# Optimization experiments

Measured on AMD Instinct MI355X. Metric: run time of the kernel, lower is better.

Reference implementation:

```python
import jax, jax.numpy as jnp
import numpy as np

S, T, I = 4096, 64, 64          # spatial cells, timesteps, input features
EH, E, H = 128, 256, 512        # embedding hidden, embedding size, LSTM hidden
LG, O, F1, F2 = 32, 128, 256, 64


def setup_inputs() -> dict:
    key = jax.random.key(0)
    ks = jax.random.split(key, 24)
    w = lambda k, shape: jax.random.normal(k, shape, jnp.float32) * 0.05
    return {
        "inputData": jax.random.normal(ks[0], (S, T, I), jnp.float32),
        "lane": jax.random.uniform(ks[1], (1, 1), jnp.float32),
        # lane gate MLP
        "Wlg1": w(ks[2], (LG, 1)),  "blg1": w(ks[3], (LG,)),
        "Wlg2": w(ks[4], (1, LG)),  "blg2": w(ks[5], (1,)),
        # embedding MLP
        "We1": w(ks[6], (EH, I)),   "be1": w(ks[7], (EH,)),
        "We2": w(ks[8], (E, EH)),   "be2": w(ks[9], (E,)),
        # LSTMCell params (torch layout: [4H, in]/[4H, H], gate order i,f,g,o)
        "Wih": w(ks[10], (4 * H, E)), "bih": w(ks[11], (4 * H,)),
        "Whh": w(ks[12], (4 * H, H)), "bhh": w(ks[13], (4 * H,)),
        # output head
        "Wout": w(ks[14], (O, H)),  "bout": w(ks[15], (O,)),
        "Wf1": w(ks[16], (F1, O)),  "bf1": w(ks[17], (F1,)),
        "Wf2": w(ks[18], (F2, F1)), "bf2": w(ks[19], (F2,)),
        "Wf3": w(ks[20], (1, F2)),  "bf3": w(ks[21], (1,)),
    }


def _spatial_maxpool(h):
    # MaxPool1d(kernel=3, stride=1, padding=1) over the spatial axis (axis 0),
    # implicit -inf padding as in torch maxpool.
    hp = jnp.pad(h, ((1, 1), (0, 0)), constant_values=-jnp.inf)
    return jnp.maximum(jnp.maximum(hp[:-2], hp[1:-1]), hp[2:])


def reference(inputData, lane, Wlg1, blg1, Wlg2, blg2, We1, be1, We2, be2,
              Wih, bih, Whh, bhh, Wout, bout, Wf1, bf1, Wf2, bf2, Wf3, bf3):
    # lane gate -> scalar in (0,1)
    lg = jax.nn.relu(lane @ Wlg1.T + blg1)
    laneC = jax.nn.sigmoid(lg @ Wlg2.T + blg2)          # [1,1]
    x = inputData * laneC.reshape(1, 1, 1)              # [S,T,I]
    # embedding MLP
    x = jax.nn.relu(x @ We1.T + be1)
    x = jax.nn.relu(x @ We2.T + be2)                    # [S,T,E]
    xt = jnp.transpose(x, (1, 0, 2))                    # [T,S,E]

    def step(carry, x_t):
        h, c = carry
        gates = x_t @ Wih.T + bih + h @ Whh.T + bhh     # [S,4H]
        i, f, g, o = jnp.split(gates, 4, axis=-1)
        c = jax.nn.sigmoid(f) * c + jax.nn.sigmoid(i) * jnp.tanh(g)
        h = jax.nn.sigmoid(o) * jnp.tanh(c)
        h = _spatial_maxpool(h)
        return (h, c), None

    h0 = jnp.zeros((inputData.shape[0], H), jnp.float32)
    c0 = jnp.zeros((inputData.shape[0], H), jnp.float32)
    (h, c), _ = jax.lax.scan(step, (h0, c0), xt)

    out = h @ Wout.T + bout
    out = jax.nn.relu(out @ Wf1.T + bf1)
    out = jax.nn.relu(out @ Wf2.T + bf2)
    out = out @ Wf3.T + bf3                             # [S,1]
    out = out / laneC.reshape(-1, 1)
    return (out, h, c)
```

## Files before the change

### kernel.cpp

```cpp
#include <hip/hip_runtime.h>
#include <hip/hip_bf16.h>
#include <cstdint>
#include <cstddef>

using bf16 = __hip_bfloat16;

typedef __attribute__((ext_vector_type(8))) short s8vec;
typedef __attribute__((ext_vector_type(4))) float f4vec;

#define SD 4096
#define TD 64
#define ID 64
#define EHD 128
#define ED 256
#define HD 512
#define GD 2048
#define OD 128
#define F1D 256
#define F2D 64

__device__ __forceinline__ float sigmf(float x) { return 1.0f / (1.0f + __expf(-x)); }
__device__ __forceinline__ float tanh_fast(float x) { return 1.0f - 2.0f / (__expf(2.0f * x) + 1.0f); }

__device__ __forceinline__ void async16(const bf16* g, void* lds) {
    __builtin_amdgcn_global_load_lds(
        (const __attribute__((address_space(1))) void*)g,
        (__attribute__((address_space(3))) void*)lds, 16, 0, 0);
}

constexpr int MODE_BF16 = 0;
constexpr int MODE_SCATTER = 2;
constexpr int MODE_LSTM = 3;

template <int MODE>
__global__ __launch_bounds__(256, 2)
void gemm_kernel(const bf16* __restrict__ A1, int lda1,
                 const bf16* __restrict__ A2, int lda2, int ksplit,
                 const bf16* __restrict__ B, int ldb,
                 const float* __restrict__ bias,
                 const float* __restrict__ scale,
                 int relu, void* __restrict__ Cp, int ldc,
                 int K, int ncols,
                 const float* __restrict__ c_in, float* __restrict__ c_out,
                 bf16* __restrict__ h_pre)
{
    __shared__ __align__(16) bf16 As[128 * 64];
    __shared__ __align__(16) bf16 Bs[128 * 64];

    const int tid = threadIdx.x;
    const int lane = tid & 63;
    const int w = tid >> 6;
    const int wm = w & 1, wn = w >> 1;
    const int m0 = blockIdx.x * 128, n0 = blockIdx.y * 128;
    const int lm = lane & 15, lq = lane >> 4;

    f4vec acc[4][4];
#pragma unroll
    for (int i = 0; i < 4; ++i)
#pragma unroll
        for (int j = 0; j < 4; ++j) acc[i][j] = (f4vec){0.f, 0.f, 0.f, 0.f};

    for (int kc = 0; kc < K; kc += 64) {
        const bf16* Ab;
        int Alda, kk;
        if (kc < ksplit) { Ab = A1; Alda = lda1; kk = kc; }
        else             { Ab = A2; Alda = lda2; kk = kc - ksplit; }

#pragma unroll
        for (int it = 0; it < 4; ++it) {
            int flat = it * 256 + tid;
            int row = flat >> 3, colu = flat & 7;
            const bf16* ga = Ab + (size_t)(m0 + row) * Alda + kk + colu * 8;
            const bf16* gb = B + (size_t)(n0 + row) * ldb + kc + colu * 8;
            uint32_t off = (uint32_t)(it * 256 + (tid & ~63)) * 16u;
            async16(ga, (char*)As + off);
            async16(gb, (char*)Bs + off);
        }
        __syncthreads();

#pragma unroll
        for (int ks = 0; ks < 64; ks += 32) {
            s8vec af[4], bfr[4];
#pragma unroll
            for (int mi = 0; mi < 4; ++mi)
                af[mi] = *(const s8vec*)(As + (wm * 64 + mi * 16 + lm) * 64 + ks + lq * 8);
#pragma unroll
            for (int ni = 0; ni < 4; ++ni)
                bfr[ni] = *(const s8vec*)(Bs + (wn * 64 + ni * 16 + lm) * 64 + ks + lq * 8);
#pragma unroll
            for (int mi = 0; mi < 4; ++mi)
#pragma unroll
                for (int ni = 0; ni < 4; ++ni)
                    acc[mi][ni] = __builtin_amdgcn_mfma_f32_16x16x32_bf16(af[mi], bfr[ni], acc[mi][ni], 0, 0, 0);
        }
        __syncthreads();
    }

    if constexpr (MODE == MODE_LSTM) {
        const int j = (n0 >> 2) + wn * 16 + lm;
        const float bi = bias[n0 + wn * 64 + lm];
        const float bff = bias[n0 + wn * 64 + 16 + lm];
        const float bg = bias[n0 + wn * 64 + 32 + lm];
        const float bo = bias[n0 + wn * 64 + 48 + lm];
#pragma unroll
        for (int mi = 0; mi < 4; ++mi) {
#pragma unroll
            for (int r = 0; r < 4; ++r) {
                const int row = m0 + wm * 64 + mi * 16 + lq * 4 + r;
                float gi = acc[mi][0][r] + bi;
                float gf = acc[mi][1][r] + bff;
                float gg = acc[mi][2][r] + bg;
                float go = acc[mi][3][r] + bo;
                float cn = sigmf(gf) * c_in[(size_t)row * HD + j] + sigmf(gi) * tanh_fast(gg);
                c_out[(size_t)row * HD + j] = cn;
                h_pre[(size_t)row * HD + j] = __float2bfloat16(sigmf(go) * tanh_fast(cn));
            }
        }
        return;
    }

    const float sc = scale ? scale[0] : 1.0f;
#pragma unroll
    for (int mi = 0; mi < 4; ++mi) {
#pragma unroll
        for (int ni = 0; ni < 4; ++ni) {
            const int gcol = n0 + wn * 64 + ni * 16 + lm;
            const float bv = bias[gcol];
#pragma unroll
            for (int r = 0; r < 4; ++r) {
                const int grow = m0 + wm * 64 + mi * 16 + lq * 4 + r;
                float v = acc[mi][ni][r] * sc + bv;
                if (relu) v = fmaxf(v, 0.f);
                if constexpr (MODE == MODE_BF16) {
                    if (gcol < ncols)
                        ((bf16*)Cp)[(size_t)grow * ldc + gcol] = __float2bfloat16(v);
                } else {
                    const int crow = (grow & 63) * SD + (grow >> 6);
                    ((bf16*)Cp)[(size_t)crow * ldc + gcol] = __float2bfloat16(v);
                }
            }
        }
    }
}

__global__ void prep_kernel(const float* __restrict__ Wih, const float* __restrict__ Whh,
                            const float* __restrict__ bih, const float* __restrict__ bhh,
                            const float* __restrict__ We1, const float* __restrict__ We2,
                            const float* __restrict__ Wout, const float* __restrict__ Wf1,
                            const float* __restrict__ Wf2, const float* __restrict__ bf2,
                            bf16* __restrict__ Wpack, float* __restrict__ biasg,
                            bf16* __restrict__ We1b, bf16* __restrict__ We2b,
                            bf16* __restrict__ Woutb, bf16* __restrict__ Wf1b,
                            bf16* __restrict__ Wf2p, float* __restrict__ bf2f)
{
    int idx = blockIdx.x * 256 + threadIdx.x;
    const int S0 = GD * (ED + HD);
    if (idx < S0) {
        int p = idx / (ED + HD), k = idx - p * (ED + HD);
        int q = p & 127;
        int j = (p >> 7) * 32 + ((q >> 6) << 4) + (q & 15);
        int gate = (q >> 4) & 3;
        int orig = gate * HD + j;
        float v = (k < ED) ? Wih[(size_t)orig * ED + k] : Whh[(size_t)orig * HD + (k - ED)];
        Wpack[idx] = __float2bfloat16(v);
        return;
    }
    idx -= S0;
    if (idx < GD) {
        int p = idx, q = p & 127;
        int j = (p >> 7) * 32 + ((q >> 6) << 4) + (q & 15);
        int gate = (q >> 4) & 3;
        int orig = gate * HD + j;
        biasg[p] = bih[orig] + bhh[orig];
        return;
    }
    idx -= GD;
    if (idx < EHD * ID) { We1b[idx] = __float2bfloat16(We1[idx]); return; }
    idx -= EHD * ID;
    if (idx < ED * EHD) { We2b[idx] = __float2bfloat16(We2[idx]); return; }
    idx -= ED * EHD;
    if (idx < OD * HD) { Woutb[idx] = __float2bfloat16(Wout[idx]); return; }
    idx -= OD * HD;
    if (idx < F1D * OD) { Wf1b[idx] = __float2bfloat16(Wf1[idx]); return; }
    idx -= F1D * OD;
    if (idx < 128 * F1D) {
        int nrow = idx >> 8;
        Wf2p[idx] = (nrow < F2D) ? __float2bfloat16(Wf2[idx]) : __float2bfloat16(0.f);
        return;
    }
    idx -= 128 * F1D;
    if (idx < 128) { bf2f[idx] = (idx < F2D) ? bf2[idx] : 0.f; return; }
}

__global__ void cvt_input_kernel(const float* __restrict__ src, bf16* __restrict__ dst)
{
    int i = (blockIdx.x * 256 + threadIdx.x) * 8;
    float4 a = *(const float4*)(src + i);
    float4 b = *(const float4*)(src + i + 4);
    bf16 o[8] = { __float2bfloat16(a.x), __float2bfloat16(a.y),
                  __float2bfloat16(a.z), __float2bfloat16(a.w),
                  __float2bfloat16(b.x), __float2bfloat16(b.y),
                  __float2bfloat16(b.z), __float2bfloat16(b.w) };
    *(uint4*)(dst + i) = *(const uint4*)o;
}

__global__ void lane_kernel(const float* __restrict__ lane, const float* __restrict__ Wlg1,
                            const float* __restrict__ blg1, const float* __restrict__ Wlg2,
                            const float* __restrict__ blg2, float* __restrict__ laneC)
{
    if (threadIdx.x != 0) return;
    const float l = lane[0];
    float acc = blg2[0];
    for (int k = 0; k < 32; ++k)
        acc += fmaxf(l * Wlg1[k] + blg1[k], 0.f) * Wlg2[k];
    float v = 1.f / (1.f + __expf(-acc));
    laneC[0] = v;
    laneC[1] = 1.f / v;
}

__global__ void zero_kernel(float* __restrict__ c0, bf16* __restrict__ h)
{
    int idx = blockIdx.x * 256 + threadIdx.x;
    if (idx < SD * HD) { c0[idx] = 0.f; h[idx] = __float2bfloat16(0.f); }
}

__global__ void maxpool_kernel(const bf16* __restrict__ hp, bf16* __restrict__ hout)
{
    int base = (blockIdx.x * 256 + threadIdx.x) * 8;
    int s = base >> 9;
    const uint4 vm = *(const uint4*)(hp + base);
    const unsigned short* m = (const unsigned short*)&vm;
    uint4 vu, vd;
    const unsigned short* u = nullptr; const unsigned short* d = nullptr;
    if (s > 0)      { vu = *(const uint4*)(hp + base - HD); u = (const unsigned short*)&vu; }
    if (s < SD - 1) { vd = *(const uint4*)(hp + base + HD); d = (const unsigned short*)&vd; }
    unsigned short o[8];
#pragma unroll
    for (int e = 0; e < 8; ++e) {
        float v = __bfloat162float(__ushort_as_bfloat16(m[e]));
        if (u) v = fmaxf(v, __bfloat162float(__ushort_as_bfloat16(u[e])));
        if (d) v = fmaxf(v, __bfloat162float(__ushort_as_bfloat16(d[e])));
        o[e] = __bfloat16_as_ushort(__float2bfloat16(v));
    }
    *(uint4*)(hout + base) = *(const uint4*)o;
}

__global__ void f3_kernel(const bf16* __restrict__ xf2, const float* __restrict__ Wf3,
                          const float* __restrict__ bf3, const float* __restrict__ laneC,
                          float* __restrict__ out)
{
    int s = blockIdx.x * 256 + threadIdx.x;
    if (s >= SD) return;
    float acc = bf3[0];
#pragma unroll
    for (int k = 0; k < F2D; ++k)
        acc += __bfloat162float(xf2[(size_t)s * F2D + k]) * Wf3[k];
    out[s] = acc * laneC[1];
}

__global__ void finalize_kernel(const bf16* __restrict__ h, const float* __restrict__ c,
                                float* __restrict__ out)
{
    int idx = blockIdx.x * 256 + threadIdx.x;
    if (idx >= SD * HD) return;
    out[SD + idx] = __bfloat162float(h[idx]);
    out[SD + SD * HD + idx] = c[idx];
}

extern "C" void kernel_launch(void* const* d_in, const int* in_sizes, int n_in,
                              void* d_out, int out_size, void* d_ws, size_t ws_size,
                              hipStream_t stream)
{
    (void)in_sizes; (void)n_in; (void)out_size;
    const float* inputDataF = (const float*)d_in[0];
    const float* lane = (const float*)d_in[1];
    const float* Wlg1 = (const float*)d_in[2];
    const float* blg1 = (const float*)d_in[3];
    const float* Wlg2 = (const float*)d_in[4];
    const float* blg2 = (const float*)d_in[5];
    const float* We1 = (const float*)d_in[6];
    const float* be1 = (const float*)d_in[7];
    const float* We2 = (const float*)d_in[8];
    const float* be2 = (const float*)d_in[9];
    const float* Wih = (const float*)d_in[10];
    const float* bih = (const float*)d_in[11];
    const float* Whh = (const float*)d_in[12];
    const float* bhh = (const float*)d_in[13];
    const float* Wout = (const float*)d_in[14];
    const float* bout = (const float*)d_in[15];
    const float* Wf1 = (const float*)d_in[16];
    const float* bf1 = (const float*)d_in[17];
    const float* Wf2 = (const float*)d_in[18];
    const float* bf2 = (const float*)d_in[19];
    const float* Wf3 = (const float*)d_in[20];
    const float* bf3 = (const float*)d_in[21];
    float* out = (float*)d_out;

    char* wp = (char*)d_ws;
    auto carve = [&](size_t bytes) { char* p = wp; wp += (bytes + 255) & ~(size_t)255; return p; };

    bf16* inb   = (bf16*)carve((size_t)SD * TD * ID * 2);
    float* laneCbuf = (float*)carve(2 * sizeof(float));
    float* cbuf0 = (float*)carve((size_t)SD * HD * 4);
    float* cbuf1 = (float*)carve((size_t)SD * HD * 4);
    bf16* hbuf  = (bf16*)carve((size_t)SD * HD * 2);
    bf16* hpre  = (bf16*)carve((size_t)SD * HD * 2);
    bf16* Wpack = (bf16*)carve((size_t)GD * (ED + HD) * 2);
    float* biasg = (float*)carve(GD * 4);
    float* bf2f = (float*)carve(128 * 4);
    bf16* We1b  = (bf16*)carve((size_t)EHD * ID * 2);
    bf16* We2b  = (bf16*)carve((size_t)ED * EHD * 2);
    bf16* Woutb = (bf16*)carve((size_t)OD * HD * 2);
    bf16* Wf1b  = (bf16*)carve((size_t)F1D * OD * 2);
    bf16* Wf2p  = (bf16*)carve((size_t)128 * F1D * 2);
    bf16* out_o = (bf16*)carve((size_t)SD * OD * 2);
    bf16* xf1   = (bf16*)carve((size_t)SD * F1D * 2);
    bf16* xf2   = (bf16*)carve((size_t)SD * F2D * 2);

    const size_t SZ_X1 = (size_t)SD * TD * EHD * 2;
    const size_t SZ_X2 = (size_t)SD * TD * ED * 2;
    const size_t used = (size_t)(wp - (char*)d_ws);
    const size_t remain = (ws_size > used) ? (ws_size - used) : 0;
    const bool persist = remain >= (SZ_X1 + SZ_X2 + 4096);

    bf16* x1 = nullptr; bf16* x2 = nullptr;
    bf16* x1t = nullptr; bf16* x2t = nullptr;
    if (persist) {
        x1 = (bf16*)carve(SZ_X1);
        x2 = (bf16*)carve(SZ_X2);
    } else {
        x1t = (bf16*)carve((size_t)SD * EHD * 2);
        x2t = (bf16*)carve((size_t)SD * ED * 2);
    }

    const int NOSPLIT = 1 << 30;
    const int PREP_N = GD * (ED + HD) + GD + EHD * ID + ED * EHD + OD * HD
                     + F1D * OD + 128 * F1D + 128;

    cvt_input_kernel<<<SD * TD * ID / (256 * 8), 256, 0, stream>>>(inputDataF, inb);
    prep_kernel<<<(PREP_N + 255) / 256, 256, 0, stream>>>(
        Wih, Whh, bih, bhh, We1, We2, Wout, Wf1, Wf2, bf2,
        Wpack, biasg, We1b, We2b, Woutb, Wf1b, Wf2p, bf2f);
    lane_kernel<<<1, 64, 0, stream>>>(lane, Wlg1, blg1, Wlg2, blg2, laneCbuf);
    zero_kernel<<<SD * HD / 256, 256, 0, stream>>>(cbuf0, hbuf);

    if (persist) {
        gemm_kernel<MODE_BF16><<<dim3(SD * TD / 128, 1), 256, 0, stream>>>(
            inb, ID, nullptr, 0, NOSPLIT, We1b, ID, be1, laneCbuf, 1,
            x1, EHD, ID, EHD, nullptr, nullptr, nullptr);
        gemm_kernel<MODE_SCATTER><<<dim3(SD * TD / 128, ED / 128), 256, 0, stream>>>(
            x1, EHD, nullptr, 0, NOSPLIT, We2b, EHD, be2, nullptr, 1,
            x2, ED, EHD, ED, nullptr, nullptr, nullptr);
    }

    for (int t = 0; t < TD; ++t) {
        const float* c_in = (t & 1) ? cbuf1 : cbuf0;
        float* c_out = (t & 1) ? cbuf0 : cbuf1;
        const bf16* xA;
        if (persist) {
            xA = x2 + (size_t)t * SD * ED;
        } else {
            gemm_kernel<MODE_BF16><<<dim3(SD / 128, 1), 256, 0, stream>>>(
                inb + (size_t)t * ID, TD * ID, nullptr, 0, NOSPLIT,
                We1b, ID, be1, laneCbuf, 1, x1t, EHD, ID, EHD,
                nullptr, nullptr, nullptr);
            gemm_kernel<MODE_BF16><<<dim3(SD / 128, ED / 128), 256, 0, stream>>>(
                x1t, EHD, nullptr, 0, NOSPLIT, We2b, EHD, be2, nullptr, 1,
                x2t, ED, EHD, ED, nullptr, nullptr, nullptr);
            xA = x2t;
        }
        gemm_kernel<MODE_LSTM><<<dim3(SD / 128, GD / 128), 256, 0, stream>>>(
            xA, ED, hbuf, HD, ED,
            Wpack, ED + HD, biasg, nullptr, 0, nullptr, 0, ED + HD, GD,
            c_in, c_out, hpre);
        maxpool_kernel<<<SD * HD / (256 * 8), 256, 0, stream>>>(hpre, hbuf);
    }

    gemm_kernel<MODE_BF16><<<dim3(SD / 128, 1), 256, 0, stream>>>(
        hbuf, HD, nullptr, 0, NOSPLIT, Woutb, HD, bout, nullptr, 0,
        out_o, OD, HD, OD, nullptr, nullptr, nullptr);
    gemm_kernel<MODE_BF16><<<dim3(SD / 128, F1D / 128), 256, 0, stream>>>(
        out_o, OD, nullptr, 0, NOSPLIT, Wf1b, OD, bf1, nullptr, 1,
        xf1, F1D, OD, F1D, nullptr, nullptr, nullptr);
    gemm_kernel<MODE_BF16><<<dim3(SD / 128, 1), 256, 0, stream>>>(
        xf1, F1D, nullptr, 0, NOSPLIT, Wf2p, F1D, bf2f, nullptr, 1,
        xf2, F2D, F1D, F2D, nullptr, nullptr, nullptr);
    f3_kernel<<<SD / 256, 256, 0, stream>>>(xf2, Wf3, bf3, laneCbuf, out);
    finalize_kernel<<<SD * HD / 256, 256, 0, stream>>>(hbuf, cbuf0, out);
}
```

Before: 2.444 ms.

## Split LSTM step GEMM into dedicated 128x64-tile kernel with repacked gate weights

Moves the per-timestep LSTM gate GEMM out of the generic templated kernel into a dedicated kernel. The new kernel uses 128x64 tiles with four warps along M, half the B tile in LDS, fewer accumulators, and launch bounds allowing four blocks per CU. The gate-interleaved weight and bias packing is changed to match the 64-wide N tile. The grid doubles to 1024 blocks per step, which fills the GPU better and raises occupancy, at the cost of loading the A tile twice as often. The finalize kernel is also vectorized to handle four elements per thread.

```diff
diff --git a/kernel.cpp b/kernel.cpp
--- a/kernel.cpp
+++ b/kernel.cpp
@@ -28,21 +28,103 @@
         (__attribute__((address_space(3))) void*)lds, 16, 0, 0);
 }
 
+__global__ __launch_bounds__(256, 4)
+void lstm_gemm(const bf16* __restrict__ xt,
+               const bf16* __restrict__ h,
+               const bf16* __restrict__ Wpack,
+               const float* __restrict__ biasg,
+               const float* __restrict__ c_in,
+               float* __restrict__ c_out,
+               bf16* __restrict__ h_pre)
+{
+    __shared__ __align__(16) bf16 As[128 * 64];
+    __shared__ __align__(16) bf16 Bs[64 * 64];
+
+    const int tid = threadIdx.x;
+    const int lane = tid & 63;
+    const int wm = tid >> 6;
+    const int m0 = blockIdx.x * 128, n0 = blockIdx.y * 64;
+    const int lm = lane & 15, lq = lane >> 4;
+
+    f4vec acc[2][4];
+#pragma unroll
+    for (int i = 0; i < 2; ++i)
+#pragma unroll
+        for (int j = 0; j < 4; ++j) acc[i][j] = (f4vec){0.f, 0.f, 0.f, 0.f};
+
+    for (int kc = 0; kc < ED + HD; kc += 64) {
+        const bf16* Ab; int Alda, kk;
+        if (kc < ED) { Ab = xt; Alda = ED; kk = kc; }
+        else         { Ab = h;  Alda = HD; kk = kc - ED; }
+
+#pragma unroll
+        for (int it = 0; it < 4; ++it) {
+            int flat = it * 256 + tid;
+            int row = flat >> 3, colu = flat & 7;
+            const bf16* ga = Ab + (size_t)(m0 + row) * Alda + kk + colu * 8;
+            uint32_t off = (uint32_t)(it * 256 + (tid & ~63)) * 16u;
+            async16(ga, (char*)As + off);
+        }
+#pragma unroll
+        for (int it = 0; it < 2; ++it) {
+            int flat = it * 256 + tid;
+            int row = flat >> 3, colu = flat & 7;
+            const bf16* gb = Wpack + (size_t)(n0 + row) * (ED + HD) + kc + colu * 8;
+            uint32_t off = (uint32_t)(it * 256 + (tid & ~63)) * 16u;
+            async16(gb, (char*)Bs + off);
+        }
+        __syncthreads();
+
+#pragma unroll
+        for (int ks = 0; ks < 64; ks += 32) {
+            s8vec af[2], bfr[4];
+#pragma unroll
+            for (int mi = 0; mi < 2; ++mi)
+                af[mi] = *(const s8vec*)(As + (wm * 32 + mi * 16 + lm) * 64 + ks + lq * 8);
+#pragma unroll
+            for (int ni = 0; ni < 4; ++ni)
+                bfr[ni] = *(const s8vec*)(Bs + (ni * 16 + lm) * 64 + ks + lq * 8);
+#pragma unroll
+            for (int mi = 0; mi < 2; ++mi)
+#pragma unroll
+                for (int ni = 0; ni < 4; ++ni)
+                    acc[mi][ni] = __builtin_amdgcn_mfma_f32_16x16x32_bf16(af[mi], bfr[ni], acc[mi][ni], 0, 0, 0);
+        }
+        __syncthreads();
+    }
+
+    const int j = (n0 >> 2) + lm;
+    const float bi = biasg[n0 + lm];
+    const float bff = biasg[n0 + 16 + lm];
+    const float bg = biasg[n0 + 32 + lm];
+    const float bo = biasg[n0 + 48 + lm];
+#pragma unroll
+    for (int mi = 0; mi < 2; ++mi) {
+#pragma unroll
+        for (int r = 0; r < 4; ++r) {
+            const int row = m0 + wm * 32 + mi * 16 + lq * 4 + r;
+            float gi = acc[mi][0][r] + bi;
+            float gf = acc[mi][1][r] + bff;
+            float gg = acc[mi][2][r] + bg;
+            float go = acc[mi][3][r] + bo;
+            float cn = sigmf(gf) * c_in[(size_t)row * HD + j] + sigmf(gi) * tanh_fast(gg);
+            c_out[(size_t)row * HD + j] = cn;
+            h_pre[(size_t)row * HD + j] = __float2bfloat16(sigmf(go) * tanh_fast(cn));
+        }
+    }
+}
+
 constexpr int MODE_BF16 = 0;
 constexpr int MODE_SCATTER = 2;
-constexpr int MODE_LSTM = 3;
 
 template <int MODE>
 __global__ __launch_bounds__(256, 2)
 void gemm_kernel(const bf16* __restrict__ A1, int lda1,
-                 const bf16* __restrict__ A2, int lda2, int ksplit,
                  const bf16* __restrict__ B, int ldb,
                  const float* __restrict__ bias,
                  const float* __restrict__ scale,
                  int relu, void* __restrict__ Cp, int ldc,
-                 int K, int ncols,
-                 const float* __restrict__ c_in, float* __restrict__ c_out,
-                 bf16* __restrict__ h_pre)
+                 int K, int ncols)
 {
     __shared__ __align__(16) bf16 As[128 * 64];
     __shared__ __align__(16) bf16 Bs[128 * 64];
@@ -61,16 +143,11 @@
         for (int j = 0; j < 4; ++j) acc[i][j] = (f4vec){0.f, 0.f, 0.f, 0.f};
 
     for (int kc = 0; kc < K; kc += 64) {
-        const bf16* Ab;
-        int Alda, kk;
-        if (kc < ksplit) { Ab = A1; Alda = lda1; kk = kc; }
-        else             { Ab = A2; Alda = lda2; kk = kc - ksplit; }
-
 #pragma unroll
         for (int it = 0; it < 4; ++it) {
             int flat = it * 256 + tid;
             int row = flat >> 3, colu = flat & 7;
-            const bf16* ga = Ab + (size_t)(m0 + row) * Alda + kk + colu * 8;
+            const bf16* ga = A1 + (size_t)(m0 + row) * lda1 + kc + colu * 8;
             const bf16* gb = B + (size_t)(n0 + row) * ldb + kc + colu * 8;
             uint32_t off = (uint32_t)(it * 256 + (tid & ~63)) * 16u;
             async16(ga, (char*)As + off);
@@ -94,29 +171,6 @@
                     acc[mi][ni] = __builtin_amdgcn_mfma_f32_16x16x32_bf16(af[mi], bfr[ni], acc[mi][ni], 0, 0, 0);
         }
         __syncthreads();
-    }
-
-    if constexpr (MODE == MODE_LSTM) {
-        const int j = (n0 >> 2) + wn * 16 + lm;
-        const float bi = bias[n0 + wn * 64 + lm];
-        const float bff = bias[n0 + wn * 64 + 16 + lm];
-        const float bg = bias[n0 + wn * 64 + 32 + lm];
-        const float bo = bias[n0 + wn * 64 + 48 + lm];
-#pragma unroll
-        for (int mi = 0; mi < 4; ++mi) {
-#pragma unroll
-            for (int r = 0; r < 4; ++r) {
-                const int row = m0 + wm * 64 + mi * 16 + lq * 4 + r;
-                float gi = acc[mi][0][r] + bi;
-                float gf = acc[mi][1][r] + bff;
-                float gg = acc[mi][2][r] + bg;
-                float go = acc[mi][3][r] + bo;
-                float cn = sigmf(gf) * c_in[(size_t)row * HD + j] + sigmf(gi) * tanh_fast(gg);
-                c_out[(size_t)row * HD + j] = cn;
-                h_pre[(size_t)row * HD + j] = __float2bfloat16(sigmf(go) * tanh_fast(cn));
-            }
-        }
-        return;
     }
 
     const float sc = scale ? scale[0] : 1.0f;
@@ -157,9 +211,8 @@
     const int S0 = GD * (ED + HD);
     if (idx < S0) {
         int p = idx / (ED + HD), k = idx - p * (ED + HD);
-        int q = p & 127;
-        int j = (p >> 7) * 32 + ((q >> 6) << 4) + (q & 15);
-        int gate = (q >> 4) & 3;
+        int gate = (p >> 4) & 3;
+        int j = (p >> 6) * 16 + (p & 15);
         int orig = gate * HD + j;
         float v = (k < ED) ? Wih[(size_t)orig * ED + k] : Whh[(size_t)orig * HD + (k - ED)];
         Wpack[idx] = __float2bfloat16(v);
@@ -167,9 +220,9 @@
     }
     idx -= S0;
     if (idx < GD) {
-        int p = idx, q = p & 127;
-        int j = (p >> 7) * 32 + ((q >> 6) << 4) + (q & 15);
-        int gate = (q >> 4) & 3;
+        int p = idx;
+        int gate = (p >> 4) & 3;
+        int j = (p >> 6) * 16 + (p & 15);
         int orig = gate * HD + j;
         biasg[p] = bih[orig] + bhh[orig];
         return;
@@ -261,10 +314,16 @@
 __global__ void finalize_kernel(const bf16* __restrict__ h, const float* __restrict__ c,
                                 float* __restrict__ out)
 {
-    int idx = blockIdx.x * 256 + threadIdx.x;
+    int idx = (blockIdx.x * 256 + threadIdx.x) * 4;
     if (idx >= SD * HD) return;
-    out[SD + idx] = __bfloat162float(h[idx]);
-    out[SD + SD * HD + idx] = c[idx];
+    uint2 hv4 = *(const uint2*)(h + idx);
+    const unsigned short* hu = (const unsigned short*)&hv4;
+    float4 hf = { __bfloat162float(__ushort_as_bfloat16(hu[0])),
+                  __bfloat162float(__ushort_as_bfloat16(hu[1])),
+                  __bfloat162float(__ushort_as_bfloat16(hu[2])),
+                  __bfloat162float(__ushort_as_bfloat16(hu[3])) };
+    *(float4*)(out + SD + idx) = hf;
+    *(float4*)(out + SD + SD * HD + idx) = *(const float4*)(c + idx);
 }
 
 extern "C" void kernel_launch(void* const* d_in, const int* in_sizes, int n_in,
@@ -333,7 +392,6 @@
         x2t = (bf16*)carve((size_t)SD * ED * 2);
     }
 
-    const int NOSPLIT = 1 << 30;
     const int PREP_N = GD * (ED + HD) + GD + EHD * ID + ED * EHD + OD * HD
                      + F1D * OD + 128 * F1D + 128;
 
@@ -346,11 +404,9 @@
 
     if (persist) {
         gemm_kernel<MODE_BF16><<<dim3(SD * TD / 128, 1), 256, 0, stream>>>(
-            inb, ID, nullptr, 0, NOSPLIT, We1b, ID, be1, laneCbuf, 1,
-            x1, EHD, ID, EHD, nullptr, nullptr, nullptr);
+            inb, ID, We1b, ID, be1, laneCbuf, 1, x1, EHD, ID, EHD);
         gemm_kernel<MODE_SCATTER><<<dim3(SD * TD / 128, ED / 128), 256, 0, stream>>>(
-            x1, EHD, nullptr, 0, NOSPLIT, We2b, EHD, be2, nullptr, 1,
-            x2, ED, EHD, ED, nullptr, nullptr, nullptr);
+            x1, EHD, We2b, EHD, be2, nullptr, 1, x2, ED, EHD, ED);
     }
 
     for (int t = 0; t < TD; ++t) {
@@ -361,30 +417,23 @@
             xA = x2 + (size_t)t * SD * ED;
         } else {
             gemm_kernel<MODE_BF16><<<dim3(SD / 128, 1), 256, 0, stream>>>(
-                inb + (size_t)t * ID, TD * ID, nullptr, 0, NOSPLIT,
-                We1b, ID, be1, laneCbuf, 1, x1t, EHD, ID, EHD,
-                nullptr, nullptr, nullptr);
+                inb + (size_t)t * ID, TD * ID, We1b, ID, be1, laneCbuf, 1,
+                x1t, EHD, ID, EHD);
             gemm_kernel<MODE_BF16><<<dim3(SD / 128, ED / 128), 256, 0, stream>>>(
-                x1t, EHD, nullptr, 0, NOSPLIT, We2b, EHD, be2, nullptr, 1,
-                x2t, ED, EHD, ED, nullptr, nullptr, nullptr);
+                x1t, EHD, We2b, EHD, be2, nullptr, 1, x2t, ED, EHD, ED);
             xA = x2t;
         }
-        gemm_kernel<MODE_LSTM><<<dim3(SD / 128, GD / 128), 256, 0, stream>>>(
-            xA, ED, hbuf, HD, ED,
-            Wpack, ED + HD, biasg, nullptr, 0, nullptr, 0, ED + HD, GD,
-            c_in, c_out, hpre);
+        lstm_gemm<<<dim3(SD / 128, GD / 64), 256, 0, stream>>>(
+            xA, hbuf, Wpack, biasg, c_in, c_out, hpre);
         maxpool_kernel<<<SD * HD / (256 * 8), 256, 0, stream>>>(hpre, hbuf);
     }
 
     gemm_kernel<MODE_BF16><<<dim3(SD / 128, 1), 256, 0, stream>>>(
-        hbuf, HD, nullptr, 0, NOSPLIT, Woutb, HD, bout, nullptr, 0,
-        out_o, OD, HD, OD, nullptr, nullptr, nullptr);
+        hbuf, HD, Woutb, HD, bout, nullptr, 0, out_o, OD, HD, OD);
     gemm_kernel<MODE_BF16><<<dim3(SD / 128, F1D / 128), 256, 0, stream>>>(
-        out_o, OD, nullptr, 0, NOSPLIT, Wf1b, OD, bf1, nullptr, 1,
-        xf1, F1D, OD, F1D, nullptr, nullptr, nullptr);
+        out_o, OD, Wf1b, OD, bf1, nullptr, 1, xf1, F1D, OD, F1D);
     gemm_kernel<MODE_BF16><<<dim3(SD / 128, 1), 256, 0, stream>>>(
-        xf1, F1D, nullptr, 0, NOSPLIT, Wf2p, F1D, bf2f, nullptr, 1,
-        xf2, F2D, F1D, F2D, nullptr, nullptr, nullptr);
+        xf1, F1D, Wf2p, F1D, bf2f, nullptr, 1, xf2, F2D, F1D, F2D);
     f3_kernel<<<SD / 256, 256, 0, stream>>>(xf2, Wf3, bf3, laneCbuf, out);
-    finalize_kernel<<<SD * HD / 256, 256, 0, stream>>>(hbuf, cbuf0, out);
-}
+    finalize_kernel<<<SD * HD / (256 * 4), 256, 0, stream>>>(hbuf, cbuf0, out);
+}
```

Measured after the change: 2.466 ms. No clear change (+0.9%).
